# Performance work log

Measured on AMD Instinct MI355X. Metric: run time of the kernel, lower is better.

The kernel has to match this reference:

```python
import jax, jax.numpy as jnp
import numpy as np

B, S, H = 64, 2048, 512


def setup_inputs() -> dict:
    key = jax.random.key(0)
    k1, k2, k3, k4, k5 = jax.random.split(key, 5)
    scale = 1.0 / np.sqrt(H)
    return {
        "decoder_hidden": jax.random.normal(k1, (B, H), dtype=jnp.float32),
        "encoder_outputs": jax.random.normal(k2, (B, S, H), dtype=jnp.float32),
        "W_q": jax.random.normal(k3, (H, H), dtype=jnp.float32) * scale,
        "W_k": jax.random.normal(k4, (H, H), dtype=jnp.float32) * scale,
        "v": jax.random.normal(k5, (H,), dtype=jnp.float32) * scale,
    }


def reference(decoder_hidden, encoder_outputs, W_q, W_k, v):
    # query: [B,H] -> [B,1,H]; torch Linear computes x @ W.T
    query = (decoder_hidden @ W_q.T)[:, None, :]          # [B,1,H]
    keys = jnp.einsum('bsh,gh->bsg', encoder_outputs, W_k)  # [B,S,H]
    energy = jnp.tanh(query + keys)                        # [B,S,H]
    scores = jnp.einsum('bsh,h->bs', energy, v)            # [B,S]
    attention_weights = jax.nn.softmax(scores, axis=1)     # [B,S]
    context = jnp.einsum('bs,bsh->bh', attention_weights, encoder_outputs)
    return context, attention_weights
```

## Files before the change

kernel.cpp:

```cpp
#include <hip/hip_runtime.h>
#include <hip/hip_bf16.h>
#include <cstdint>


typedef __attribute__((ext_vector_type(8))) short short8;
typedef __attribute__((ext_vector_type(4))) float f32x4;

__device__ __forceinline__ unsigned short f2bf(float f) {
    unsigned u = __builtin_bit_cast(unsigned, f);
    u += 0x7FFFu + ((u >> 16) & 1u);
    return (unsigned short)(u >> 16);
}

__device__ __forceinline__ float tanh_fast(float x) {
    float e = __expf(2.0f * x);
    return 1.0f - 2.0f * __builtin_amdgcn_rcpf(e + 1.0f);
}

__device__ __forceinline__ void async16(const unsigned short* g, short* l) {
    __builtin_amdgcn_global_load_lds(
        (const __attribute__((address_space(1))) unsigned int*)g,
        (__attribute__((address_space(3))) unsigned int*)l, 16, 0, 0);
}

__global__ void cast_wk_kernel(const float* __restrict__ wk, unsigned short* __restrict__ wkb) {
    int i = (blockIdx.x * 256 + threadIdx.x) * 4;
    float4 f = *(const float4*)(wk + i);
    ushort4 o;
    o.x = f2bf(f.x); o.y = f2bf(f.y); o.z = f2bf(f.z); o.w = f2bf(f.w);
    *(ushort4*)(wkb + i) = o;
}

__global__ void q_kernel(const float* __restrict__ dec, const float* __restrict__ wq,
                         float* __restrict__ q) {
    int b  = blockIdx.x >> 3;
    int g0 = (blockIdx.x & 7) * 64;
    int t = threadIdx.x, lane = t & 63, w = t >> 6;
    __shared__ float dls[512];
    dls[t] = dec[b * 512 + t];
    dls[t + 256] = dec[b * 512 + 256 + t];
    __syncthreads();
    #pragma unroll
    for (int gi = 0; gi < 16; ++gi) {
        int g = g0 + w + gi * 4;
        float acc = 0.f;
        #pragma unroll
        for (int it = 0; it < 2; ++it) {
            int h = (it * 64 + lane) * 4;
            float4 wv = *(const float4*)(wq + (size_t)g * 512 + h);
            acc += wv.x * dls[h] + wv.y * dls[h + 1] + wv.z * dls[h + 2] + wv.w * dls[h + 3];
        }
        #pragma unroll
        for (int m = 32; m; m >>= 1) acc += __shfl_xor(acc, m, 64);
        if (lane == 0) q[b * 512 + g] = acc;
    }
}

__launch_bounds__(256, 2)
__global__ void scores_kernel(const float* __restrict__ enc, const unsigned short* __restrict__ wkb,
                              const float* __restrict__ q, const float* __restrict__ v,
                              float* __restrict__ scores) {
    __shared__ __align__(16) short Bs[512 * 32];
    __shared__ __align__(16) short As[64 * 40];
    __shared__ float q_s[512];
    __shared__ float v_s[512];
    __shared__ float red[4][64];

    int t = threadIdx.x, lane = t & 63, w = t >> 6;
    int quad = lane >> 4, l15 = lane & 15;
    int tile = blockIdx.x;
    int b = tile >> 5;
    size_t m0 = (size_t)tile * 64;

    q_s[t] = q[b * 512 + t];   q_s[t + 256] = q[b * 512 + 256 + t];
    v_s[t] = v[t];             v_s[t + 256] = v[t + 256];

    f32x4 acc[4][8];
    #pragma unroll
    for (int i = 0; i < 4; ++i)
        #pragma unroll
        for (int j = 0; j < 8; ++j)
            acc[i][j] = (f32x4){0.f, 0.f, 0.f, 0.f};

    int arow = t >> 2, akq = t & 3;
    const float* aptr = enc + (m0 + arow) * 512 + akq * 8;

    int kqs = (lane & 3) ^ ((lane >> 3) & 3);
    const unsigned short* bgbase = wkb + (size_t)(w * 16 + (lane >> 2)) * 512 + kqs * 8;
    short* blbase = &Bs[(w * 16 + (lane >> 2)) * 32 + (lane & 3) * 8];

    for (int kk = 0; kk < 512; kk += 32) {
        __syncthreads();
        #pragma unroll
        for (int i = 0; i < 8; ++i)
            async16(bgbase + (size_t)i * 64 * 512 + kk, blbase + i * 64 * 32);
        float4 fa0 = *(const float4*)(aptr + kk);
        float4 fa1 = *(const float4*)(aptr + kk + 4);
        short8 av;
        av[0] = (short)f2bf(fa0.x); av[1] = (short)f2bf(fa0.y);
        av[2] = (short)f2bf(fa0.z); av[3] = (short)f2bf(fa0.w);
        av[4] = (short)f2bf(fa1.x); av[5] = (short)f2bf(fa1.y);
        av[6] = (short)f2bf(fa1.z); av[7] = (short)f2bf(fa1.w);
        *(short8*)&As[arow * 40 + akq * 8] = av;
        __syncthreads();

        short8 af[4];
        #pragma unroll
        for (int mt = 0; mt < 4; ++mt)
            af[mt] = *(short8*)&As[(mt * 16 + l15) * 40 + quad * 8];
        #pragma unroll
        for (int nt = 0; nt < 8; ++nt) {
            int brow = w * 128 + nt * 16 + l15;
            short8 bf = *(short8*)&Bs[brow * 32 + (quad ^ ((l15 >> 1) & 3)) * 8];
            #pragma unroll
            for (int mt = 0; mt < 4; ++mt)
                acc[mt][nt] = __builtin_amdgcn_mfma_f32_16x16x32_bf16(af[mt], bf, acc[mt][nt], 0, 0, 0);
        }
    }

    float rs[4][4];
    #pragma unroll
    for (int mt = 0; mt < 4; ++mt)
        #pragma unroll
        for (int r = 0; r < 4; ++r) rs[mt][r] = 0.f;
    #pragma unroll
    for (int nt = 0; nt < 8; ++nt) {
        int g = w * 128 + nt * 16 + l15;
        float qb = q_s[g], vv = v_s[g];
        #pragma unroll
        for (int mt = 0; mt < 4; ++mt)
            #pragma unroll
            for (int r = 0; r < 4; ++r)
                rs[mt][r] += tanh_fast(qb + acc[mt][nt][r]) * vv;
    }
    #pragma unroll
    for (int m = 1; m <= 8; m <<= 1)
        #pragma unroll
        for (int mt = 0; mt < 4; ++mt)
            #pragma unroll
            for (int r = 0; r < 4; ++r)
                rs[mt][r] += __shfl_xor(rs[mt][r], m, 64);
    if (l15 == 0) {
        #pragma unroll
        for (int mt = 0; mt < 4; ++mt)
            #pragma unroll
            for (int r = 0; r < 4; ++r)
                red[w][mt * 16 + quad * 4 + r] = rs[mt][r];
    }
    __syncthreads();
    if (t < 64) {
        float sc = red[0][t] + red[1][t] + red[2][t] + red[3][t];
        scores[m0 + t] = sc;
    }
}

__global__ void softmax_kernel(float* __restrict__ out) {
    int b = blockIdx.x, t = threadIdx.x, lane = t & 63, w = t >> 6;
    float* sc = out + 32768 + b * 2048;
    __shared__ float wred[4];
    float vals[8];
    float mx = -1e30f;
    #pragma unroll
    for (int i = 0; i < 8; ++i) { vals[i] = sc[t + i * 256]; mx = fmaxf(mx, vals[i]); }
    #pragma unroll
    for (int m = 32; m; m >>= 1) mx = fmaxf(mx, __shfl_xor(mx, m, 64));
    if (lane == 0) wred[w] = mx;
    __syncthreads();
    mx = fmaxf(fmaxf(wred[0], wred[1]), fmaxf(wred[2], wred[3]));
    __syncthreads();
    float s = 0.f;
    #pragma unroll
    for (int i = 0; i < 8; ++i) { vals[i] = __expf(vals[i] - mx); s += vals[i]; }
    #pragma unroll
    for (int m = 32; m; m >>= 1) s += __shfl_xor(s, m, 64);
    if (lane == 0) wred[w] = s;
    __syncthreads();
    s = wred[0] + wred[1] + wred[2] + wred[3];
    float inv = 1.0f / s;
    #pragma unroll
    for (int i = 0; i < 8; ++i) sc[t + i * 256] = vals[i] * inv;
    out[b * 512 + t] = 0.f;
    out[b * 512 + 256 + t] = 0.f;
}

__launch_bounds__(256)
__global__ void context_kernel(const float* __restrict__ enc, float* __restrict__ out) {
    int blk = blockIdx.x;
    int b = blk >> 5, rem = blk & 31, hc = rem >> 4, ss = rem & 15;
    int t = threadIdx.x, lane = t & 63, sg = t >> 6;
    int h = hc * 256 + lane * 4;
    const float* wptr = out + 32768 + b * 2048;
    float ax = 0.f, ay = 0.f, az = 0.f, aw = 0.f;
    int sbase = ss * 128 + sg;
    #pragma unroll 8
    for (int i = 0; i < 32; ++i) {
        int s = sbase + i * 4;
        float wv = wptr[s];
        float4 e = *(const float4*)(enc + ((size_t)b * 2048 + s) * 512 + h);
        ax += wv * e.x; ay += wv * e.y; az += wv * e.z; aw += wv * e.w;
    }
    __shared__ float red[4][64][4];
    red[sg][lane][0] = ax; red[sg][lane][1] = ay; red[sg][lane][2] = az; red[sg][lane][3] = aw;
    __syncthreads();
    if (t < 64) {
        float* dst = out + b * 512 + hc * 256 + t * 4;
        #pragma unroll
        for (int j = 0; j < 4; ++j) {
            float sv = red[0][t][j] + red[1][t][j] + red[2][t][j] + red[3][t][j];
            atomicAdd(dst + j, sv);
        }
    }
}

extern "C" void kernel_launch(void* const* d_in, const int* in_sizes, int n_in,
                              void* d_out, int out_size, void* d_ws, size_t ws_size,
                              hipStream_t stream) {
    const float* dec = (const float*)d_in[0];
    const float* enc = (const float*)d_in[1];
    const float* wq  = (const float*)d_in[2];
    const float* wk  = (const float*)d_in[3];
    const float* v   = (const float*)d_in[4];
    float* out = (float*)d_out;

    unsigned short* wkb = (unsigned short*)d_ws;
    float* q = (float*)((char*)d_ws + 512 * 512 * 2);

    cast_wk_kernel<<<256, 256, 0, stream>>>(wk, wkb);
    q_kernel<<<512, 256, 0, stream>>>(dec, wq, q);
    scores_kernel<<<2048, 256, 0, stream>>>(enc, wkb, q, v, out + 32768);
    softmax_kernel<<<64, 256, 0, stream>>>(out);
    context_kernel<<<2048, 256, 0, stream>>>(enc, out);
}
```

Measured before the change: 468.6 us.

## Double-buffer LDS tiles in scores GEMM and prefetch encoder loads

Converts the scores kernel's K loop into a two-stage pipeline. The next W_k tile is loaded asynchronously into a second LDS buffer and the encoder rows are prefetched into registers two steps ahead, so there is one barrier per iteration instead of two. The q and v values are moved from LDS into per-thread registers. LDS use per block roughly doubles (about 75KB), which may cut occupancy below the two blocks per CU requested by launch bounds, and register pressure rises.

```diff
diff --git a/kernel.cpp b/kernel.cpp
--- a/kernel.cpp
+++ b/kernel.cpp
@@ -60,10 +60,8 @@
 __global__ void scores_kernel(const float* __restrict__ enc, const unsigned short* __restrict__ wkb,
                               const float* __restrict__ q, const float* __restrict__ v,
                               float* __restrict__ scores) {
-    __shared__ __align__(16) short Bs[512 * 32];
-    __shared__ __align__(16) short As[64 * 40];
-    __shared__ float q_s[512];
-    __shared__ float v_s[512];
+    __shared__ __align__(16) short Bs[2][512 * 32];
+    __shared__ __align__(16) short As[2][64 * 40];
     __shared__ float red[4][64];
 
     int t = threadIdx.x, lane = t & 63, w = t >> 6;
@@ -72,8 +70,13 @@
     int b = tile >> 5;
     size_t m0 = (size_t)tile * 64;
 
-    q_s[t] = q[b * 512 + t];   q_s[t + 256] = q[b * 512 + 256 + t];
-    v_s[t] = v[t];             v_s[t + 256] = v[t + 256];
+    float q_g[8], v_g[8];
+    #pragma unroll
+    for (int nt = 0; nt < 8; ++nt) {
+        int g = w * 128 + nt * 16 + l15;
+        q_g[nt] = q[b * 512 + g];
+        v_g[nt] = v[g];
+    }
 
     f32x4 acc[4][8];
     #pragma unroll
@@ -87,35 +90,64 @@
 
     int kqs = (lane & 3) ^ ((lane >> 3) & 3);
     const unsigned short* bgbase = wkb + (size_t)(w * 16 + (lane >> 2)) * 512 + kqs * 8;
-    short* blbase = &Bs[(w * 16 + (lane >> 2)) * 32 + (lane & 3) * 8];
-
-    for (int kk = 0; kk < 512; kk += 32) {
-        __syncthreads();
-        #pragma unroll
-        for (int i = 0; i < 8; ++i)
-            async16(bgbase + (size_t)i * 64 * 512 + kk, blbase + i * 64 * 32);
-        float4 fa0 = *(const float4*)(aptr + kk);
-        float4 fa1 = *(const float4*)(aptr + kk + 4);
+    short* bl[2];
+    bl[0] = &Bs[0][(w * 16 + (lane >> 2)) * 32 + (lane & 3) * 8];
+    bl[1] = &Bs[1][(w * 16 + (lane >> 2)) * 32 + (lane & 3) * 8];
+
+    #pragma unroll
+    for (int i = 0; i < 8; ++i)
+        async16(bgbase + (size_t)i * 64 * 512, bl[0] + i * 64 * 32);
+    {
+        float4 fa0 = *(const float4*)(aptr);
+        float4 fa1 = *(const float4*)(aptr + 4);
         short8 av;
         av[0] = (short)f2bf(fa0.x); av[1] = (short)f2bf(fa0.y);
         av[2] = (short)f2bf(fa0.z); av[3] = (short)f2bf(fa0.w);
         av[4] = (short)f2bf(fa1.x); av[5] = (short)f2bf(fa1.y);
         av[6] = (short)f2bf(fa1.z); av[7] = (short)f2bf(fa1.w);
-        *(short8*)&As[arow * 40 + akq * 8] = av;
-        __syncthreads();
+        *(short8*)&As[0][arow * 40 + akq * 8] = av;
+    }
+    float4 pa0 = *(const float4*)(aptr + 32);
+    float4 pa1 = *(const float4*)(aptr + 36);
+    __syncthreads();
+
+    #pragma unroll 2
+    for (int kk = 0; kk < 512; kk += 32) {
+        int buf = (kk >> 5) & 1, nbuf = buf ^ 1;
+        if (kk < 480) {
+            #pragma unroll
+            for (int i = 0; i < 8; ++i)
+                async16(bgbase + (size_t)i * 64 * 512 + kk + 32, bl[nbuf] + i * 64 * 32);
+        }
+        float4 na0, na1;
+        if (kk < 448) {
+            na0 = *(const float4*)(aptr + kk + 64);
+            na1 = *(const float4*)(aptr + kk + 68);
+        }
 
         short8 af[4];
         #pragma unroll
         for (int mt = 0; mt < 4; ++mt)
-            af[mt] = *(short8*)&As[(mt * 16 + l15) * 40 + quad * 8];
+            af[mt] = *(short8*)&As[buf][(mt * 16 + l15) * 40 + quad * 8];
         #pragma unroll
         for (int nt = 0; nt < 8; ++nt) {
             int brow = w * 128 + nt * 16 + l15;
-            short8 bf = *(short8*)&Bs[brow * 32 + (quad ^ ((l15 >> 1) & 3)) * 8];
+            short8 bf = *(short8*)&Bs[buf][brow * 32 + (quad ^ ((l15 >> 1) & 3)) * 8];
             #pragma unroll
             for (int mt = 0; mt < 4; ++mt)
                 acc[mt][nt] = __builtin_amdgcn_mfma_f32_16x16x32_bf16(af[mt], bf, acc[mt][nt], 0, 0, 0);
         }
+
+        if (kk < 480) {
+            short8 av;
+            av[0] = (short)f2bf(pa0.x); av[1] = (short)f2bf(pa0.y);
+            av[2] = (short)f2bf(pa0.z); av[3] = (short)f2bf(pa0.w);
+            av[4] = (short)f2bf(pa1.x); av[5] = (short)f2bf(pa1.y);
+            av[6] = (short)f2bf(pa1.z); av[7] = (short)f2bf(pa1.w);
+            *(short8*)&As[nbuf][arow * 40 + akq * 8] = av;
+            pa0 = na0; pa1 = na1;
+        }
+        __syncthreads();
     }
 
     float rs[4][4];
@@ -125,8 +157,7 @@
         for (int r = 0; r < 4; ++r) rs[mt][r] = 0.f;
     #pragma unroll
     for (int nt = 0; nt < 8; ++nt) {
-        int g = w * 128 + nt * 16 + l15;
-        float qb = q_s[g], vv = v_s[g];
+        float qb = q_g[nt], vv = v_g[nt];
         #pragma unroll
         for (int mt = 0; mt < 4; ++mt)
             #pragma unroll
```

New measurement: 470.6 us. Within noise of the previous version (+0.4%).
